# Kernel tuning notes

Measured on AMD Instinct MI355X. Metric: run time of the kernel, lower is better.

The kernel has to match this reference:

```python
import jax, jax.numpy as jnp
import numpy as np

B, C, L = 256, 512, 150
CI = C // 4            # channel_in = in_dim // 4 = 128
K = 150                # one_hot_cls_num (depthwise kernel over length)
POOL = 150             # MaxPool2d kernel (150, 1)
EPS = 1e-5             # BatchNorm eps


def setup_inputs() -> dict:
    key = jax.random.key(0)
    ks = jax.random.split(key, 8)
    n = lambda k, shape, s: jax.random.normal(k, shape, jnp.float32) * s
    return {
        "x":    jax.random.normal(ks[0], (B, C, L, 1), jnp.float32),
        "Wv":   n(ks[1], (CI, C), 0.06),   "bv": jnp.zeros((CI,), jnp.float32),
        "Wq":   n(ks[2], (CI, CI), 0.12),  "bq": jnp.zeros((CI,), jnp.float32),
        "Wk":   n(ks[3], (CI, CI), 0.12),  "bk": jnp.zeros((CI,), jnp.float32),
        "gamma": n(ks[4], (), 1.0),
        "Wd":   n(ks[5], (2 * CI, K), 0.1), "bd": jnp.zeros((2 * CI,), jnp.float32),
        "Wp":   n(ks[6], (2 * CI, 2 * CI), 0.08), "bp": jnp.zeros((2 * CI,), jnp.float32),
        "bn_g": jnp.ones((2 * CI,), jnp.float32),
        "bn_b": jnp.zeros((2 * CI,), jnp.float32),
    }


def reference(x, Wv, bv, Wq, bq, Wk, bk, gamma, Wd, bd, Wp, bp, bn_g, bn_b):
    xb = x[..., 0]                                             # [B, C, L] (trailing width==1)
    # 1x1 convs are per-position matmuls over the channel dim
    v = jnp.einsum('oc,bcl->bol', Wv, xb) + bv[:, None]        # [B, CI, L]
    q = jnp.einsum('oc,bcl->bol', Wq, v) + bq[:, None]         # [B, CI, L]
    k = jnp.einsum('oc,bcl->bol', Wk, v) + bk[:, None]         # [B, CI, L]
    # raw (unscaled) attention: energy = q^T k, softmax over keys
    energy = jnp.einsum('bci,bcj->bij', q, k)                  # [B, L, L]
    attn = jax.nn.softmax(energy, axis=-1)
    # x = bmm(v, attn^T): out[b,c,i] = sum_j v[b,c,j] * attn[b,i,j]
    att_out = jnp.einsum('bcj,bij->bci', v, attn)              # [B, CI, L]
    cat = jnp.concatenate([gamma * att_out, v], axis=1)        # [B, 2CI, L]
    # MaxPool2d kernel=(150,1), stride=(150,1) over length
    Lp = L // POOL
    y = cat[:, :, : Lp * POOL].reshape(B, 2 * CI, Lp, POOL).max(axis=-1)
    y = y.reshape(B, -1)                                       # [B, 2CI*Lp]
    # depthwise conv kernel (K,1), VALID padding, groups = 2CI
    dw = jax.lax.conv_general_dilated(
        cat[:, :, :, None],                                    # [B, 2CI, L, 1]
        Wd[:, None, :, None],                                  # [2CI, 1, K, 1]
        window_strides=(1, 1), padding='VALID',
        dimension_numbers=('NCHW', 'OIHW', 'NCHW'),
        feature_group_count=2 * CI,
    ) + bd[None, :, None, None]                                # [B, 2CI, L-K+1, 1]
    # pointwise 1x1 conv
    pw = jnp.einsum('oc,bchw->bohw', Wp, dw) + bp[None, :, None, None]
    # BatchNorm2d in training mode: per-channel batch stats (biased variance)
    mean = pw.mean(axis=(0, 2, 3))
    var = pw.var(axis=(0, 2, 3))
    xn = (pw - mean[None, :, None, None]) * jax.lax.rsqrt(var[None, :, None, None] + EPS)
    out = jax.nn.relu(xn * bn_g[None, :, None, None] + bn_b[None, :, None, None])
    return jnp.concatenate([out.reshape(B, -1), y], axis=1)    # [B, 2CI*(L-K+1) + 2CI*Lp]
```

## Files before the change

kernel.cpp:

```cpp
#include <hip/hip_runtime.h>


typedef float f32x4  __attribute__((ext_vector_type(4)));
typedef float f32x16 __attribute__((ext_vector_type(16)));
typedef short s16x8  __attribute__((ext_vector_type(8)));
typedef unsigned short BF;

union U8 { s16x8 v; BF u[8]; uint2 d[2]; unsigned w[4]; };

__device__ __forceinline__ BF bfhi(float f) { return (BF)(__float_as_uint(f) >> 16); }
__device__ __forceinline__ float bff(BF h) { return __uint_as_float(((unsigned)h) << 16); }
__device__ __forceinline__ BF bflo(float f, BF hi) { return bfhi(f - bff(hi)); }
__device__ __forceinline__ BF bfrne(float f) {
    unsigned u = __float_as_uint(f);
    u += 0x7fffu + ((u >> 16) & 1u);
    return (BF)(u >> 16);
}
__device__ __forceinline__ s16x8 ld8l(const BF* p) {
    U8 t; t.d[0] = *(const uint2*)p; t.d[1] = *(const uint2*)(p + 4); return t.v;
}
__device__ __forceinline__ void st4(BF* p, BF a, BF b, BF c, BF d) {
    uint2 t; t.x = (unsigned)a | ((unsigned)b << 16);
    t.y = (unsigned)c | ((unsigned)d << 16);
    *(uint2*)p = t;
}
__device__ __forceinline__ void ldv8(const unsigned* p, s16x8& hi, s16x8& lo) {
    unsigned u[8];
    *(uint4*)&u[0] = *(const uint4*)p;
    *(uint4*)&u[4] = *(const uint4*)(p + 4);
    U8 H, L;
    #pragma unroll
    for (int e = 0; e < 4; ++e) {
        unsigned a = u[2*e], b2 = u[2*e + 1];
        H.w[e] = (a >> 16) | (b2 & 0xffff0000u);
        L.w[e] = (a & 0xffffu) | (b2 << 16);
    }
    hi = H.v; lo = L.v;
}
#define MFMA(a, b, c)   __builtin_amdgcn_mfma_f32_16x16x32_bf16(a, b, c, 0, 0, 0)
#define MFMA32(a, b, c) __builtin_amdgcn_mfma_f32_32x32x16_bf16(a, b, c, 0, 0, 0)

__global__ __launch_bounds__(256)
void prep_all(const float* __restrict__ Wv, const float* __restrict__ Wq,
              const float* __restrict__ Wk, const float* __restrict__ bq,
              BF* __restrict__ wvh, BF* __restrict__ wvl,
              BF* __restrict__ wqh, BF* __restrict__ wql,
              float* __restrict__ cvec)
{
    __shared__ float qs[128][33], ks_[128][33];
    const int blk = blockIdx.x, tid = threadIdx.x;
    if (blk < 64) {
        int i = blk * 1024 + tid * 4;
        float4 v = *(const float4*)(Wv + i);
        BF h0 = bfhi(v.x), h1 = bfhi(v.y), h2 = bfhi(v.z), h3 = bfhi(v.w);
        st4(&wvh[i], h0, h1, h2, h3);
        st4(&wvl[i], bflo(v.x,h0), bflo(v.y,h1), bflo(v.z,h2), bflo(v.w,h3));
    } else if (blk < 80) {
        int bi = blk - 64;
        int d1_0 = (bi >> 2) * 32, d2_0 = (bi & 3) * 32;
        for (int i = tid; i < 4096; i += 256) {
            int o = i >> 5, c = i & 31;
            qs[o][c]  = Wq[o * 128 + d1_0 + c];
            ks_[o][c] = Wk[o * 128 + d2_0 + c];
        }
        __syncthreads();
        #pragma unroll
        for (int j = 0; j < 4; ++j) {
            int idx = j * 256 + tid;
            int d1 = idx >> 5, d2 = idx & 31;
            float s = 0.f;
            #pragma unroll 8
            for (int o = 0; o < 128; ++o) s = fmaf(qs[o][d1], ks_[o][d2], s);
            BF h = bfhi(s);
            wqh[(d1_0 + d1) * 128 + d2_0 + d2] = h;
            wql[(d1_0 + d1) * 128 + d2_0 + d2] = bflo(s, h);
        }
    } else {
        if (tid < 128) {
            float s = 0.f;
            for (int o = 0; o < 128; ++o) s += bq[o] * Wk[o * 128 + tid];
            cvec[tid] = s;
        }
    }
}

__global__ __launch_bounds__(512, 4)
void k1_v(const float* __restrict__ x, const BF* __restrict__ wvh,
          const BF* __restrict__ wvl, const float* __restrict__ bv,
          const float* __restrict__ Wd,
          unsigned* __restrict__ vp, float* __restrict__ vpm,
          float* __restrict__ vpd)
{
    __shared__ BF xt[2][2][80][36];
    const int bx = blockIdx.x;
    const int b = bx & 255, lh = bx >> 8;
    const int l0 = lh * 80;
    const float* xb = x + (long)b * 76800 + l0;
    const int tid = threadIdx.x, lane = tid & 63, w = tid >> 6;
    const int li = lane & 15, gq = lane >> 4;

    if (w < 4) {
        f32x4 acc[5][2];
        #pragma unroll
        for (int mf = 0; mf < 5; ++mf)
            #pragma unroll
            for (int nf = 0; nf < 2; ++nf) acc[mf][nf] = f32x4{0.f,0.f,0.f,0.f};
        s16x8 bh[2], bl[2];
        #pragma unroll
        for (int nf = 0; nf < 2; ++nf) {
            long g = (long)(w*32 + nf*16 + li)*512 + gq*8;
            bh[nf] = *(const s16x8*)(wvh + g);
            bl[nf] = *(const s16x8*)(wvl + g);
        }
        __syncthreads();
        for (int p = 0; p < 16; ++p) {
            s16x8 nbh[2], nbl[2];
            if (p < 15) {
                #pragma unroll
                for (int nf = 0; nf < 2; ++nf) {
                    long g = (long)(w*32 + nf*16 + li)*512 + (p+1)*32 + gq*8;
                    nbh[nf] = *(const s16x8*)(wvh + g);
                    nbl[nf] = *(const s16x8*)(wvl + g);
                }
            }
            const BF (*xh)[36] = xt[p & 1][0];
            const BF (*xl)[36] = xt[p & 1][1];
            #pragma unroll
            for (int mf = 0; mf < 5; ++mf) {
                int row = mf*16 + li;
                s16x8 ah = ld8l(&xh[row][gq*8]);
                s16x8 al = ld8l(&xl[row][gq*8]);
                #pragma unroll
                for (int nf = 0; nf < 2; ++nf) {
                    acc[mf][nf] = MFMA(al, bh[nf], acc[mf][nf]);
                    acc[mf][nf] = MFMA(ah, bl[nf], acc[mf][nf]);
                    acc[mf][nf] = MFMA(ah, bh[nf], acc[mf][nf]);
                }
            }
            if (p < 15) {
                #pragma unroll
                for (int nf = 0; nf < 2; ++nf) { bh[nf] = nbh[nf]; bl[nf] = nbl[nf]; }
            }
            __syncthreads();
        }
        #pragma unroll
        for (int nf = 0; nf < 2; ++nf) {
            int c = w*32 + nf*16 + li;
            float bvv = bv[c];
            float mx = -3.4e38f, dt = 0.f;
            #pragma unroll
            for (int mf = 0; mf < 5; ++mf)
                #pragma unroll
                for (int r = 0; r < 4; ++r) {
                    int ll = mf*16 + gq*4 + r;
                    float f = acc[mf][nf][r] + bvv;
                    BF h = bfhi(f);
                    BF lo2 = bflo(f, h);
                    vp[((long)b*160 + l0 + ll)*128 + c] = ((unsigned)h << 16) | lo2;
                    if (l0 + ll < 150) {
                        mx = fmaxf(mx, f);
                        dt = fmaf(f, Wd[(128 + c)*150 + l0 + ll], dt);
                    }
                }
            mx = fmaxf(mx, __shfl_xor(mx, 16)); dt += __shfl_xor(dt, 16);
            mx = fmaxf(mx, __shfl_xor(mx, 32)); dt += __shfl_xor(dt, 32);
            if (gq == 0) {
                vpm[((long)lh*256 + b)*128 + c] = mx;
                vpd[((long)lh*256 + b)*128 + c] = dt;
            }
        }
    } else {
        const int sw = w - 4;
        const int bound = (lh == 0) ? 16 : 6;
        float cur[2][8];
        auto ldchunk = [&](int p) {
            #pragma unroll
            for (int cc = 0; cc < 8; ++cc) {
                int ch = p*32 + sw*8 + cc;
                cur[0][cc] = xb[ch*150 + lane];
                cur[1][cc] = (lane < bound) ? xb[ch*150 + 64 + lane] : 0.f;
            }
        };
        auto wrchunk = [&](int buf) {
            #pragma unroll
            for (int g2 = 0; g2 < 2; ++g2) {
                BF h0 = bfhi(cur[0][g2*4+0]), h1 = bfhi(cur[0][g2*4+1]);
                BF h2 = bfhi(cur[0][g2*4+2]), h3 = bfhi(cur[0][g2*4+3]);
                st4(&xt[buf][0][lane][sw*8 + g2*4], h0, h1, h2, h3);
                st4(&xt[buf][1][lane][sw*8 + g2*4],
                    bflo(cur[0][g2*4+0],h0), bflo(cur[0][g2*4+1],h1),
                    bflo(cur[0][g2*4+2],h2), bflo(cur[0][g2*4+3],h3));
                if (lane < 16) {
                    BF k0 = bfhi(cur[1][g2*4+0]), k1 = bfhi(cur[1][g2*4+1]);
                    BF k2 = bfhi(cur[1][g2*4+2]), k3 = bfhi(cur[1][g2*4+3]);
                    st4(&xt[buf][0][64 + lane][sw*8 + g2*4], k0, k1, k2, k3);
                    st4(&xt[buf][1][64 + lane][sw*8 + g2*4],
                        bflo(cur[1][g2*4+0],k0), bflo(cur[1][g2*4+1],k1),
                        bflo(cur[1][g2*4+2],k2), bflo(cur[1][g2*4+3],k3));
                }
            }
        };
        ldchunk(0); wrchunk(0); ldchunk(1);
        __syncthreads();
        for (int p = 0; p < 16; ++p) {
            if (p < 15) {
                wrchunk((p + 1) & 1);
                if (p < 14) ldchunk(p + 2);
            }
            __syncthreads();
        }
    }
}

__global__ __launch_bounds__(1024, 8)
void k2_attn(const unsigned* __restrict__ vp,
             const BF* __restrict__ wqh, const BF* __restrict__ wql,
             const float* __restrict__ cvec, const float* __restrict__ gammap,
             const float* __restrict__ Wd,
             const float* __restrict__ vpm, const float* __restrict__ vpd,
             float* __restrict__ dw, float* __restrict__ out)
{
    __shared__ char smem[60672];
    BF (*ts)[2][192][36] = (BF(*)[2][192][36])smem;
    BF (*P)[172] = (BF(*)[172])smem;
    float* smax = (float*)(smem + 55296);
    float* ssum = smax + 480;
    float* svp  = ssum + 480;

    const int b = blockIdx.x;
    const unsigned* vb = vp + (long)b * 20480;
    const int tid = threadIdx.x;
    const int lane = tid & 63, w = tid >> 6;
    const int li = lane & 15, gq = lane >> 4;
    const int l31 = lane & 31, hi5 = lane >> 5;
    const float gamma = gammap[0];

    f32x4 eacc[2][4];
    #pragma unroll
    for (int a = 0; a < 2; ++a)
        #pragma unroll
        for (int b2 = 0; b2 < 4; ++b2) eacc[a][b2] = f32x4{0.f,0.f,0.f,0.f};
    const int iw = w / 3, jw = w % 3;

    for (int pr = 0; pr < 2; ++pr) {
        if (w < 10) {
            const int s2 = w / 5, jt = w % 5;
            const int ss = pr*2 + s2;
            f32x16 tacc;
            #pragma unroll
            for (int r = 0; r < 16; ++r) tacc[r] = 0.f;
            const unsigned* arow = vb + (jt*32 + l31)*128;
            const long brow = (long)(ss*32 + l31)*128;
            #pragma unroll
            for (int kc = 0; kc < 8; ++kc) {
                int kof = kc*16 + hi5*8;
                s16x8 bh = *(const s16x8*)(wqh + brow + kof);
                s16x8 bl = *(const s16x8*)(wql + brow + kof);
                s16x8 ah, al;
                ldv8(arow + kof, ah, al);
                tacc = MFMA32(al, bh, tacc);
                tacc = MFMA32(ah, bl, tacc);
                tacc = MFMA32(ah, bh, tacc);
            }
            #pragma unroll
            for (int r = 0; r < 16; ++r) {
                int j = jt*32 + (r & 3) + 8*(r >> 2) + 4*hi5;
                float f = tacc[r];
                BF h = bfhi(f);
                ts[s2][0][j][l31] = h;
                ts[s2][1][j][l31] = bflo(f, h);
            }
        } else if (pr == 0) {
            int t2 = tid - 640;
            unsigned* tz = (unsigned*)smem;
            for (int z = t2; z < 2304; z += 384) {
                int sb = z / 576, rz = z % 576;
                tz[(sb*192 + 160)*18 + rz] = 0u;
            }
            int r = t2 >> 1, hf = t2 & 1;
            if (r < 160) {
                const unsigned* vr = vb + r*128 + hf*64;
                float s = 0.f;
                #pragma unroll 8
                for (int d2 = 0; d2 < 64; ++d2)
                    s += cvec[hf*64 + d2] * bff((BF)(vr[d2] >> 16));
                svp[hf*192 + r] = s;
            }
        }
        __syncthreads();
        if (w < 15) {
            #pragma unroll
            for (int s2 = 0; s2 < 2; ++s2) {
                int scol = (pr*2 + s2)*32 + gq*8;
                s16x8 ah[2], al[2];
                #pragma unroll
                for (int mf2 = 0; mf2 < 2; ++mf2)
                    ldv8(vb + (iw*32 + mf2*16 + li)*128 + scol, ah[mf2], al[mf2]);
                #pragma unroll
                for (int nf = 0; nf < 4; ++nf) {
                    int jr = jw*64 + nf*16 + li;
                    s16x8 bh = ld8l(&ts[s2][0][jr][gq*8]);
                    s16x8 bl = ld8l(&ts[s2][1][jr][gq*8]);
                    #pragma unroll
                    for (int mf2 = 0; mf2 < 2; ++mf2) {
                        eacc[mf2][nf] = MFMA(ah[mf2], bh, eacc[mf2][nf]);
                        eacc[mf2][nf] = MFMA(ah[mf2], bl, eacc[mf2][nf]);
                        eacc[mf2][nf] = MFMA(al[mf2], bh, eacc[mf2][nf]);
                    }
                }
            }
        }
        __syncthreads();
    }

    if (w < 15) {
        #pragma unroll
        for (int nf = 0; nf < 4; ++nf) {
            int j = jw*64 + nf*16 + li;
            float sv = svp[j] + svp[192 + j];
            #pragma unroll
            for (int mf2 = 0; mf2 < 2; ++mf2)
                #pragma unroll
                for (int r = 0; r < 4; ++r)
                    eacc[mf2][nf][r] += sv;
        }
        #pragma unroll
        for (int mf2 = 0; mf2 < 2; ++mf2)
            #pragma unroll
            for (int r = 0; r < 4; ++r) {
                int i = iw*32 + mf2*16 + gq*4 + r;
                float m = -3.4e38f;
                #pragma unroll
                for (int nf = 0; nf < 4; ++nf) {
                    int j = jw*64 + nf*16 + li;
                    if (j < 150) m = fmaxf(m, eacc[mf2][nf][r]);
                }
                #pragma unroll
                for (int o = 1; o < 16; o <<= 1) m = fmaxf(m, __shfl_xor(m, o));
                if (li == 0) smax[jw*160 + i] = m;
            }
    }
    __syncthreads();
    if (w < 15) {
        #pragma unroll
        for (int mf2 = 0; mf2 < 2; ++mf2)
            #pragma unroll
            for (int r = 0; r < 4; ++r) {
                int i = iw*32 + mf2*16 + gq*4 + r;
                float gm = fmaxf(fmaxf(smax[i], smax[160 + i]), smax[320 + i]);
                float rs_ = 0.f;
                #pragma unroll
                for (int nf = 0; nf < 4; ++nf) {
                    int j = jw*64 + nf*16 + li;
                    float e = (j < 150) ? __expf(eacc[mf2][nf][r] - gm) : 0.f;
                    eacc[mf2][nf][r] = e;
                    rs_ += e;
                }
                #pragma unroll
                for (int o = 1; o < 16; o <<= 1) rs_ += __shfl_xor(rs_, o);
                if (li == 0) ssum[jw*160 + i] = rs_;
            }
    }
    __syncthreads();
    if (w < 15) {
        #pragma unroll
        for (int mf2 = 0; mf2 < 2; ++mf2)
            #pragma unroll
            for (int r = 0; r < 4; ++r) {
                int i = iw*32 + mf2*16 + gq*4 + r;
                float inv = 1.f / (ssum[i] + ssum[160 + i] + ssum[320 + i]);
                #pragma unroll
                for (int nf = 0; nf < 4; ++nf) {
                    int j = jw*64 + nf*16 + li;
                    if (j < 160) P[i][j] = bfrne(eacc[mf2][nf][r] * inv);
                }
            }
    }
    __syncthreads();

    {
        const int pc = w & 7, pi = w >> 3;
        f32x4 oacc[5];
        #pragma unroll
        for (int i = 0; i < 5; ++i) oacc[i] = f32x4{0.f,0.f,0.f,0.f};
        #pragma unroll
        for (int ks = 0; ks < 5; ++ks) {
            int c = pc*16 + li;
            int j0 = ks*32 + gq*8;
            U8 t;
            #pragma unroll
            for (int e = 0; e < 8; ++e)
                t.u[e] = (BF)(vb[(j0 + e)*128 + c] >> 16);
            #pragma unroll
            for (int nf2 = 0; nf2 < 5; ++nf2) {
                int ir = pi*80 + nf2*16 + li;
                s16x8 bp = ld8l(&P[ir][ks*32 + gq*8]);
                oacc[nf2] = MFMA(t.v, bp, oacc[nf2]);
            }
        }

        float* pmax = smax;
        float* pdot = ssum;
        #pragma unroll
        for (int r = 0; r < 4; ++r) {
            int c = pc*16 + gq*4 + r;
            float mx = -3.4e38f, dt = 0.f;
            #pragma unroll
            for (int nf2 = 0; nf2 < 5; ++nf2) {
                int l = pi*80 + nf2*16 + li;
                if (l < 150) {
                    float val = gamma * oacc[nf2][r];
                    mx = fmaxf(mx, val);
                    dt = fmaf(val, Wd[c*150 + l], dt);
                }
            }
            #pragma unroll
            for (int o = 1; o < 16; o <<= 1) {
                mx = fmaxf(mx, __shfl_xor(mx, o));
                dt += __shfl_xor(dt, o);
            }
            if (li == 0) { pmax[pi*128 + c] = mx; pdot[pi*128 + c] = dt; }
        }
        __syncthreads();
        if (tid < 128) {
            out[(long)b*512 + 256 + tid] = fmaxf(pmax[tid], pmax[128 + tid]);
            dw[b*256 + tid] = pdot[tid] + pdot[128 + tid];
        } else if (tid < 256) {
            int c2 = tid - 128;
            float m0 = vpm[(long)b*128 + c2];
            float m1 = vpm[(long)(256 + b)*128 + c2];
            out[(long)b*512 + 384 + c2] = fmaxf(m0, m1);
            dw[b*256 + 128 + c2] = vpd[(long)b*128 + c2] + vpd[(long)(256 + b)*128 + c2];
        }
    }
}

__global__ __launch_bounds__(256)
void tail_pwbn(const float* __restrict__ dw, const float* __restrict__ Wp,
               const float* __restrict__ bn_g, const float* __restrict__ bn_b,
               float* __restrict__ out)
{
    __shared__ float wp_s[256];
    __shared__ float rs[4], rs2[4];
    const int o = blockIdx.x, t = threadIdx.x;
    const int lane = t & 63, w = t >> 6;
    wp_s[t] = Wp[o * 256 + t];
    __syncthreads();
    const float4* dr = (const float4*)(dw + (long)t * 256);
    float acc = 0.f;
    #pragma unroll 8
    for (int i = 0; i < 64; ++i) {
        float4 d4 = dr[i];
        acc = fmaf(d4.x, wp_s[i*4+0], acc);
        acc = fmaf(d4.y, wp_s[i*4+1], acc);
        acc = fmaf(d4.z, wp_s[i*4+2], acc);
        acc = fmaf(d4.w, wp_s[i*4+3], acc);
    }
    float s = acc, s2 = acc * acc;
    #pragma unroll
    for (int d = 1; d < 64; d <<= 1) { s += __shfl_xor(s, d); s2 += __shfl_xor(s2, d); }
    if (lane == 0) { rs[w] = s; rs2[w] = s2; }
    __syncthreads();
    float S  = rs[0] + rs[1] + rs[2] + rs[3];
    float S2 = rs2[0] + rs2[1] + rs2[2] + rs2[3];
    float mean = S * (1.f/256.f);
    float var  = S2 * (1.f/256.f) - mean * mean;
    float sc = rsqrtf(var + 1e-5f) * bn_g[o];
    float sh = bn_b[o] - mean * sc;
    out[(long)t * 512 + o] = fmaxf(fmaf(acc, sc, sh), 0.f);
}

extern "C" void kernel_launch(void* const* d_in, const int* in_sizes, int n_in,
                              void* d_out, int out_size, void* d_ws, size_t ws_size,
                              hipStream_t stream)
{
    (void)in_sizes; (void)n_in; (void)out_size; (void)ws_size;
    const float* x    = (const float*)d_in[0];
    const float* Wv   = (const float*)d_in[1];
    const float* bv   = (const float*)d_in[2];
    const float* Wq   = (const float*)d_in[3];
    const float* bq   = (const float*)d_in[4];
    const float* Wk   = (const float*)d_in[5];
    const float* bk   = (const float*)d_in[6];  (void)bk;
    const float* gam  = (const float*)d_in[7];
    const float* Wd   = (const float*)d_in[8];
    const float* Wp   = (const float*)d_in[10];
    const float* bn_g = (const float*)d_in[12];
    const float* bn_b = (const float*)d_in[13];
    float* out = (float*)d_out;

    char* wsb = (char*)d_ws;
    BF* wvh   = (BF*)wsb;
    BF* wvl   = (BF*)(wsb + 131072);
    BF* wqh   = (BF*)(wsb + 262144);
    BF* wql   = (BF*)(wsb + 294912);
    float* cvec = (float*)(wsb + 327680);
    unsigned* vpck = (unsigned*)(wsb + 328192);
    float* vpm  = (float*)(wsb + 21299712);
    float* vpd  = (float*)(wsb + 21561856);
    float* dw   = (float*)wsb;

    prep_all<<<81, 256, 0, stream>>>(Wv, Wq, Wk, bq, wvh, wvl, wqh, wql, cvec);
    k1_v<<<512, 512, 0, stream>>>(x, wvh, wvl, bv, Wd, vpck, vpm, vpd);
    k2_attn<<<256, 1024, 0, stream>>>(vpck, wqh, wql, cvec, gam, Wd, vpm, vpd,
                                      dw, out);
    tail_pwbn<<<256, 256, 0, stream>>>(dw, Wp, bn_g, bn_b, out);
}
```

Baseline: 107.7 us.

## Split k1 and k2 over length/query quarters, move svp to k1, add combine kernel

k1_v now processes 40-position quarters per block (1024 blocks) instead of 80-position halves, and it also computes the per-key bias term svg (v·cvec) that k2 used to compute. k2_attn is split across two query halves per batch (512 blocks), stores the transposed K operand as packed 32-bit hi/lo words, and computes the softmax in one pass with a per-segment max/sum merge. Per-half pooled max and depthwise dot partials go to global memory, and a new tail_comb kernel reduces them. The aim is more blocks for occupancy and less redundant work per block. In exchange it adds a kernel launch and extra global traffic, and each k2 block recomputes the K transpose for its half.

```diff
diff --git a/kernel.cpp b/kernel.cpp
--- a/kernel.cpp
+++ b/kernel.cpp
@@ -36,6 +36,10 @@
         L.w[e] = (a & 0xffffu) | (b2 << 16);
     }
     hi = H.v; lo = L.v;
+}
+__device__ __forceinline__ unsigned packf(float f) {
+    BF h = bfhi(f);
+    return ((unsigned)h << 16) | (unsigned)bflo(f, h);
 }
 #define MFMA(a, b, c)   __builtin_amdgcn_mfma_f32_16x16x32_bf16(a, b, c, 0, 0, 0)
 #define MFMA32(a, b, c) __builtin_amdgcn_mfma_f32_32x32x16_bf16(a, b, c, 0, 0, 0)
@@ -84,31 +88,34 @@
     }
 }
 
-__global__ __launch_bounds__(512, 4)
+__global__ __launch_bounds__(512, 8)
 void k1_v(const float* __restrict__ x, const BF* __restrict__ wvh,
           const BF* __restrict__ wvl, const float* __restrict__ bv,
-          const float* __restrict__ Wd,
-          unsigned* __restrict__ vp, float* __restrict__ vpm,
-          float* __restrict__ vpd)
+          const float* __restrict__ cvec, const float* __restrict__ Wd,
+          unsigned* __restrict__ vp, float* __restrict__ svg,
+          float* __restrict__ vpm, float* __restrict__ vpd)
 {
-    __shared__ BF xt[2][2][80][36];
+    __shared__ BF xt[2][2][48][40];
+    BF (*vhl)[132] = (BF(*)[132])&xt[0][0][0][0];
+
     const int bx = blockIdx.x;
-    const int b = bx & 255, lh = bx >> 8;
-    const int l0 = lh * 80;
-    const float* xb = x + (long)b * 76800 + l0;
+    const int b = bx & 255, lq = bx >> 8;
+    const int l0 = lq * 40;
+    const float* xb = x + (long)b * 76800;
     const int tid = threadIdx.x, lane = tid & 63, w = tid >> 6;
     const int li = lane & 15, gq = lane >> 4;
 
     if (w < 4) {
-        f32x4 acc[5][2];
-        #pragma unroll
-        for (int mf = 0; mf < 5; ++mf)
+        const int cw = w;
+        f32x4 acc[3][2];
+        #pragma unroll
+        for (int mf = 0; mf < 3; ++mf)
             #pragma unroll
             for (int nf = 0; nf < 2; ++nf) acc[mf][nf] = f32x4{0.f,0.f,0.f,0.f};
         s16x8 bh[2], bl[2];
         #pragma unroll
         for (int nf = 0; nf < 2; ++nf) {
-            long g = (long)(w*32 + nf*16 + li)*512 + gq*8;
+            long g = (long)(cw*32 + nf*16 + li)*512 + gq*8;
             bh[nf] = *(const s16x8*)(wvh + g);
             bl[nf] = *(const s16x8*)(wvl + g);
         }
@@ -118,18 +125,18 @@
             if (p < 15) {
                 #pragma unroll
                 for (int nf = 0; nf < 2; ++nf) {
-                    long g = (long)(w*32 + nf*16 + li)*512 + (p+1)*32 + gq*8;
+                    long g = (long)(cw*32 + nf*16 + li)*512 + (p+1)*32 + gq*8;
                     nbh[nf] = *(const s16x8*)(wvh + g);
                     nbl[nf] = *(const s16x8*)(wvl + g);
                 }
             }
-            const BF (*xh)[36] = xt[p & 1][0];
-            const BF (*xl)[36] = xt[p & 1][1];
-            #pragma unroll
-            for (int mf = 0; mf < 5; ++mf) {
+            const BF (*xh)[40] = xt[p & 1][0];
+            const BF (*xl)[40] = xt[p & 1][1];
+            #pragma unroll
+            for (int mf = 0; mf < 3; ++mf) {
                 int row = mf*16 + li;
-                s16x8 ah = ld8l(&xh[row][gq*8]);
-                s16x8 al = ld8l(&xl[row][gq*8]);
+                s16x8 ah = *(const s16x8*)&xh[row][gq*8];
+                s16x8 al = *(const s16x8*)&xl[row][gq*8];
                 #pragma unroll
                 for (int nf = 0; nf < 2; ++nf) {
                     acc[mf][nf] = MFMA(al, bh[nf], acc[mf][nf]);
@@ -145,58 +152,52 @@
         }
         #pragma unroll
         for (int nf = 0; nf < 2; ++nf) {
-            int c = w*32 + nf*16 + li;
+            int c = cw*32 + nf*16 + li;
             float bvv = bv[c];
             float mx = -3.4e38f, dt = 0.f;
             #pragma unroll
-            for (int mf = 0; mf < 5; ++mf)
+            for (int mf = 0; mf < 3; ++mf)
                 #pragma unroll
                 for (int r = 0; r < 4; ++r) {
                     int ll = mf*16 + gq*4 + r;
                     float f = acc[mf][nf][r] + bvv;
-                    BF h = bfhi(f);
-                    BF lo2 = bflo(f, h);
-                    vp[((long)b*160 + l0 + ll)*128 + c] = ((unsigned)h << 16) | lo2;
-                    if (l0 + ll < 150) {
-                        mx = fmaxf(mx, f);
-                        dt = fmaf(f, Wd[(128 + c)*150 + l0 + ll], dt);
+                    vhl[ll][c] = bfhi(f);
+                    if (ll < 40) {
+                        vp[((long)b*160 + l0 + ll)*128 + c] = packf(f);
+                        if (l0 + ll < 150) {
+                            mx = fmaxf(mx, f);
+                            dt = fmaf(f, Wd[(128 + c)*150 + l0 + ll], dt);
+                        }
                     }
                 }
             mx = fmaxf(mx, __shfl_xor(mx, 16)); dt += __shfl_xor(dt, 16);
             mx = fmaxf(mx, __shfl_xor(mx, 32)); dt += __shfl_xor(dt, 32);
             if (gq == 0) {
-                vpm[((long)lh*256 + b)*128 + c] = mx;
-                vpd[((long)lh*256 + b)*128 + c] = dt;
+                vpm[((long)lq*256 + b)*128 + c] = mx;
+                vpd[((long)lq*256 + b)*128 + c] = dt;
             }
         }
     } else {
         const int sw = w - 4;
-        const int bound = (lh == 0) ? 16 : 6;
-        float cur[2][8];
+        float cur[8];
+        const bool ok = (lane < 40) && (l0 + lane < 150);
         auto ldchunk = [&](int p) {
             #pragma unroll
             for (int cc = 0; cc < 8; ++cc) {
                 int ch = p*32 + sw*8 + cc;
-                cur[0][cc] = xb[ch*150 + lane];
-                cur[1][cc] = (lane < bound) ? xb[ch*150 + 64 + lane] : 0.f;
+                cur[cc] = ok ? xb[ch*150 + l0 + lane] : 0.f;
             }
         };
         auto wrchunk = [&](int buf) {
-            #pragma unroll
-            for (int g2 = 0; g2 < 2; ++g2) {
-                BF h0 = bfhi(cur[0][g2*4+0]), h1 = bfhi(cur[0][g2*4+1]);
-                BF h2 = bfhi(cur[0][g2*4+2]), h3 = bfhi(cur[0][g2*4+3]);
-                st4(&xt[buf][0][lane][sw*8 + g2*4], h0, h1, h2, h3);
-                st4(&xt[buf][1][lane][sw*8 + g2*4],
-                    bflo(cur[0][g2*4+0],h0), bflo(cur[0][g2*4+1],h1),
-                    bflo(cur[0][g2*4+2],h2), bflo(cur[0][g2*4+3],h3));
-                if (lane < 16) {
-                    BF k0 = bfhi(cur[1][g2*4+0]), k1 = bfhi(cur[1][g2*4+1]);
-                    BF k2 = bfhi(cur[1][g2*4+2]), k3 = bfhi(cur[1][g2*4+3]);
-                    st4(&xt[buf][0][64 + lane][sw*8 + g2*4], k0, k1, k2, k3);
-                    st4(&xt[buf][1][64 + lane][sw*8 + g2*4],
-                        bflo(cur[1][g2*4+0],k0), bflo(cur[1][g2*4+1],k1),
-                        bflo(cur[1][g2*4+2],k2), bflo(cur[1][g2*4+3],k3));
+            if (lane < 48) {
+                #pragma unroll
+                for (int g2 = 0; g2 < 2; ++g2) {
+                    BF h0 = bfhi(cur[g2*4+0]), h1 = bfhi(cur[g2*4+1]);
+                    BF h2 = bfhi(cur[g2*4+2]), h3 = bfhi(cur[g2*4+3]);
+                    st4(&xt[buf][0][lane][sw*8 + g2*4], h0, h1, h2, h3);
+                    st4(&xt[buf][1][lane][sw*8 + g2*4],
+                        bflo(cur[g2*4+0],h0), bflo(cur[g2*4+1],h1),
+                        bflo(cur[g2*4+2],h2), bflo(cur[g2*4+3],h3));
                 }
             }
         };
@@ -210,24 +211,37 @@
             __syncthreads();
         }
     }
+    __syncthreads();
+
+    if (tid < 320) {
+        int j = tid >> 3, ds = tid & 7;
+        float s = 0.f;
+        #pragma unroll
+        for (int k = 0; k < 16; ++k) {
+            int d = ds*16 + k;
+            s = fmaf(bff(vhl[j][d]), cvec[d], s);
+        }
+        s += __shfl_xor(s, 1); s += __shfl_xor(s, 2); s += __shfl_xor(s, 4);
+        if (ds == 0) svg[(long)b*160 + l0 + j] = s;
+    }
 }
 
 __global__ __launch_bounds__(1024, 8)
 void k2_attn(const unsigned* __restrict__ vp,
              const BF* __restrict__ wqh, const BF* __restrict__ wql,
-             const float* __restrict__ cvec, const float* __restrict__ gammap,
+             const float* __restrict__ svg, const float* __restrict__ gammap,
              const float* __restrict__ Wd,
-             const float* __restrict__ vpm, const float* __restrict__ vpd,
-             float* __restrict__ dw, float* __restrict__ out)
+             float* __restrict__ pmax_g, float* __restrict__ pdot_g)
 {
-    __shared__ char smem[60672];
-    BF (*ts)[2][192][36] = (BF(*)[2][192][36])smem;
-    BF (*P)[172] = (BF(*)[172])smem;
-    float* smax = (float*)(smem + 55296);
-    float* ssum = smax + 480;
-    float* svp  = ssum + 480;
-
-    const int b = blockIdx.x;
+    __shared__ char smem[69632];
+    unsigned (*ts32)[192][44] = (unsigned(*)[192][44])smem;
+    BF (*P)[168] = (BF(*)[168])smem;
+    float* mg = (float*)(smem + 67584);
+    float* sg = mg + 240;
+
+    const int bid = blockIdx.x;
+    const int b = bid & 255, ih = bid >> 8;
+    const int i0g = ih * 80;
     const unsigned* vb = vp + (long)b * 20480;
     const int tid = threadIdx.x;
     const int lane = tid & 63, w = tid >> 6;
@@ -235,12 +249,11 @@
     const int l31 = lane & 31, hi5 = lane >> 5;
     const float gamma = gammap[0];
 
-    f32x4 eacc[2][4];
+    const int iw = w / 3, jw = w % 3;
+
+    f32x4 eacc[4];
     #pragma unroll
-    for (int a = 0; a < 2; ++a)
-        #pragma unroll
-        for (int b2 = 0; b2 < 4; ++b2) eacc[a][b2] = f32x4{0.f,0.f,0.f,0.f};
-    const int iw = w / 3, jw = w % 3;
+    for (int i = 0; i < 4; ++i) eacc[i] = f32x4{0.f,0.f,0.f,0.f};
 
     for (int pr = 0; pr < 2; ++pr) {
         if (w < 10) {
@@ -265,26 +278,7 @@
             #pragma unroll
             for (int r = 0; r < 16; ++r) {
                 int j = jt*32 + (r & 3) + 8*(r >> 2) + 4*hi5;
-                float f = tacc[r];
-                BF h = bfhi(f);
-                ts[s2][0][j][l31] = h;
-                ts[s2][1][j][l31] = bflo(f, h);
-            }
-        } else if (pr == 0) {
-            int t2 = tid - 640;
-            unsigned* tz = (unsigned*)smem;
-            for (int z = t2; z < 2304; z += 384) {
-                int sb = z / 576, rz = z % 576;
-                tz[(sb*192 + 160)*18 + rz] = 0u;
-            }
-            int r = t2 >> 1, hf = t2 & 1;
-            if (r < 160) {
-                const unsigned* vr = vb + r*128 + hf*64;
-                float s = 0.f;
-                #pragma unroll 8
-                for (int d2 = 0; d2 < 64; ++d2)
-                    s += cvec[hf*64 + d2] * bff((BF)(vr[d2] >> 16));
-                svp[hf*192 + r] = s;
+                ts32[s2][j][l31] = packf(tacc[r]);
             }
         }
         __syncthreads();
@@ -292,21 +286,16 @@
             #pragma unroll
             for (int s2 = 0; s2 < 2; ++s2) {
                 int scol = (pr*2 + s2)*32 + gq*8;
-                s16x8 ah[2], al[2];
-                #pragma unroll
-                for (int mf2 = 0; mf2 < 2; ++mf2)
-                    ldv8(vb + (iw*32 + mf2*16 + li)*128 + scol, ah[mf2], al[mf2]);
+                s16x8 ah, al;
+                ldv8(vb + (long)(i0g + iw*16 + li)*128 + scol, ah, al);
                 #pragma unroll
                 for (int nf = 0; nf < 4; ++nf) {
                     int jr = jw*64 + nf*16 + li;
-                    s16x8 bh = ld8l(&ts[s2][0][jr][gq*8]);
-                    s16x8 bl = ld8l(&ts[s2][1][jr][gq*8]);
-                    #pragma unroll
-                    for (int mf2 = 0; mf2 < 2; ++mf2) {
-                        eacc[mf2][nf] = MFMA(ah[mf2], bh, eacc[mf2][nf]);
-                        eacc[mf2][nf] = MFMA(ah[mf2], bl, eacc[mf2][nf]);
-                        eacc[mf2][nf] = MFMA(al[mf2], bh, eacc[mf2][nf]);
-                    }
+                    s16x8 bh, bl;
+                    ldv8(&ts32[s2][jr][gq*8], bh, bl);
+                    eacc[nf] = MFMA(ah, bl, eacc[nf]);
+                    eacc[nf] = MFMA(al, bh, eacc[nf]);
+                    eacc[nf] = MFMA(ah, bh, eacc[nf]);
                 }
             }
         }
@@ -317,72 +306,61 @@
         #pragma unroll
         for (int nf = 0; nf < 4; ++nf) {
             int j = jw*64 + nf*16 + li;
-            float sv = svp[j] + svp[192 + j];
-            #pragma unroll
-            for (int mf2 = 0; mf2 < 2; ++mf2)
-                #pragma unroll
-                for (int r = 0; r < 4; ++r)
-                    eacc[mf2][nf][r] += sv;
-        }
-        #pragma unroll
-        for (int mf2 = 0; mf2 < 2; ++mf2)
-            #pragma unroll
-            for (int r = 0; r < 4; ++r) {
-                int i = iw*32 + mf2*16 + gq*4 + r;
-                float m = -3.4e38f;
-                #pragma unroll
-                for (int nf = 0; nf < 4; ++nf) {
-                    int j = jw*64 + nf*16 + li;
-                    if (j < 150) m = fmaxf(m, eacc[mf2][nf][r]);
-                }
-                #pragma unroll
-                for (int o = 1; o < 16; o <<= 1) m = fmaxf(m, __shfl_xor(m, o));
-                if (li == 0) smax[jw*160 + i] = m;
-            }
+            float sv = svg[(long)b*160 + j];
+            #pragma unroll
+            for (int r = 0; r < 4; ++r) eacc[nf][r] += sv;
+        }
+        #pragma unroll
+        for (int r = 0; r < 4; ++r) {
+            int il = iw*16 + gq*4 + r;
+            float m = -3.4e38f;
+            #pragma unroll
+            for (int nf = 0; nf < 4; ++nf) {
+                int j = jw*64 + nf*16 + li;
+                if (j < 150) m = fmaxf(m, eacc[nf][r]);
+            }
+            #pragma unroll
+            for (int o = 1; o < 16; o <<= 1) m = fmaxf(m, __shfl_xor(m, o));
+            float rs_ = 0.f;
+            #pragma unroll
+            for (int nf = 0; nf < 4; ++nf) {
+                int j = jw*64 + nf*16 + li;
+                float e = (j < 150) ? __expf(eacc[nf][r] - m) : 0.f;
+                eacc[nf][r] = e;
+                rs_ += e;
+            }
+            #pragma unroll
+            for (int o = 1; o < 16; o <<= 1) rs_ += __shfl_xor(rs_, o);
+            if (li == 0) { mg[jw*80 + il] = m; sg[jw*80 + il] = rs_; }
+        }
     }
     __syncthreads();
     if (w < 15) {
         #pragma unroll
-        for (int mf2 = 0; mf2 < 2; ++mf2)
-            #pragma unroll
-            for (int r = 0; r < 4; ++r) {
-                int i = iw*32 + mf2*16 + gq*4 + r;
-                float gm = fmaxf(fmaxf(smax[i], smax[160 + i]), smax[320 + i]);
-                float rs_ = 0.f;
-                #pragma unroll
-                for (int nf = 0; nf < 4; ++nf) {
-                    int j = jw*64 + nf*16 + li;
-                    float e = (j < 150) ? __expf(eacc[mf2][nf][r] - gm) : 0.f;
-                    eacc[mf2][nf][r] = e;
-                    rs_ += e;
-                }
-                #pragma unroll
-                for (int o = 1; o < 16; o <<= 1) rs_ += __shfl_xor(rs_, o);
-                if (li == 0) ssum[jw*160 + i] = rs_;
-            }
-    }
-    __syncthreads();
-    if (w < 15) {
-        #pragma unroll
-        for (int mf2 = 0; mf2 < 2; ++mf2)
-            #pragma unroll
-            for (int r = 0; r < 4; ++r) {
-                int i = iw*32 + mf2*16 + gq*4 + r;
-                float inv = 1.f / (ssum[i] + ssum[160 + i] + ssum[320 + i]);
-                #pragma unroll
-                for (int nf = 0; nf < 4; ++nf) {
-                    int j = jw*64 + nf*16 + li;
-                    if (j < 160) P[i][j] = bfrne(eacc[mf2][nf][r] * inv);
-                }
-            }
+        for (int r = 0; r < 4; ++r) {
+            int il = iw*16 + gq*4 + r;
+            float m0 = mg[il], m1 = mg[80 + il], m2 = mg[160 + il];
+            float M = fmaxf(fmaxf(m0, m1), m2);
+            float S = fmaf(sg[il], __expf(m0 - M),
+                      fmaf(sg[80 + il], __expf(m1 - M),
+                           sg[160 + il] * __expf(m2 - M)));
+            float scale = __expf(mg[jw*80 + il] - M) / S;
+            #pragma unroll
+            for (int nf = 0; nf < 4; ++nf) {
+                int j = jw*64 + nf*16 + li;
+                if (j < 160) P[il][j] = bfrne(eacc[nf][r] * scale);
+            }
+        }
     }
     __syncthreads();
 
     {
         const int pc = w & 7, pi = w >> 3;
-        f32x4 oacc[5];
-        #pragma unroll
-        for (int i = 0; i < 5; ++i) oacc[i] = f32x4{0.f,0.f,0.f,0.f};
+        const int nfc = pi ? 2 : 3;
+        const int ibase = pi * 48;
+        f32x4 oacc[3];
+        #pragma unroll
+        for (int i = 0; i < 3; ++i) oacc[i] = f32x4{0.f,0.f,0.f,0.f};
         #pragma unroll
         for (int ks = 0; ks < 5; ++ks) {
             int c = pc*16 + li;
@@ -390,24 +368,19 @@
             U8 t;
             #pragma unroll
             for (int e = 0; e < 8; ++e)
-                t.u[e] = (BF)(vb[(j0 + e)*128 + c] >> 16);
-            #pragma unroll
-            for (int nf2 = 0; nf2 < 5; ++nf2) {
-                int ir = pi*80 + nf2*16 + li;
+                t.u[e] = (BF)(vb[(long)(j0 + e)*128 + c] >> 16);
+            for (int nf2 = 0; nf2 < nfc; ++nf2) {
+                int ir = ibase + nf2*16 + li;
                 s16x8 bp = ld8l(&P[ir][ks*32 + gq*8]);
                 oacc[nf2] = MFMA(t.v, bp, oacc[nf2]);
             }
         }
-
-        float* pmax = smax;
-        float* pdot = ssum;
         #pragma unroll
         for (int r = 0; r < 4; ++r) {
             int c = pc*16 + gq*4 + r;
             float mx = -3.4e38f, dt = 0.f;
-            #pragma unroll
-            for (int nf2 = 0; nf2 < 5; ++nf2) {
-                int l = pi*80 + nf2*16 + li;
+            for (int nf2 = 0; nf2 < nfc; ++nf2) {
+                int l = i0g + ibase + nf2*16 + li;
                 if (l < 150) {
                     float val = gamma * oacc[nf2][r];
                     mx = fmaxf(mx, val);
@@ -419,19 +392,40 @@
                 mx = fmaxf(mx, __shfl_xor(mx, o));
                 dt += __shfl_xor(dt, o);
             }
-            if (li == 0) { pmax[pi*128 + c] = mx; pdot[pi*128 + c] = dt; }
-        }
-        __syncthreads();
-        if (tid < 128) {
-            out[(long)b*512 + 256 + tid] = fmaxf(pmax[tid], pmax[128 + tid]);
-            dw[b*256 + tid] = pdot[tid] + pdot[128 + tid];
-        } else if (tid < 256) {
-            int c2 = tid - 128;
-            float m0 = vpm[(long)b*128 + c2];
-            float m1 = vpm[(long)(256 + b)*128 + c2];
-            out[(long)b*512 + 384 + c2] = fmaxf(m0, m1);
-            dw[b*256 + 128 + c2] = vpd[(long)b*128 + c2] + vpd[(long)(256 + b)*128 + c2];
-        }
+            if (li == 0) {
+                long k = (long)(ih*2 + pi)*256 + b;
+                pmax_g[k*128 + c] = mx;
+                pdot_g[k*128 + c] = dt;
+            }
+        }
+    }
+}
+
+__global__ __launch_bounds__(256)
+void tail_comb(const float* __restrict__ pmax_g, const float* __restrict__ pdot_g,
+               const float* __restrict__ vpm, const float* __restrict__ vpd,
+               float* __restrict__ dw, float* __restrict__ out)
+{
+    const int b = blockIdx.x, ch = threadIdx.x;
+    if (ch < 128) {
+        float mx = -3.4e38f, dt = 0.f;
+        #pragma unroll
+        for (int k = 0; k < 4; ++k) {
+            mx = fmaxf(mx, pmax_g[((long)k*256 + b)*128 + ch]);
+            dt += pdot_g[((long)k*256 + b)*128 + ch];
+        }
+        out[(long)b*512 + 256 + ch] = mx;
+        dw[b*256 + ch] = dt;
+    } else {
+        int c2 = ch - 128;
+        float mx = -3.4e38f, dt = 0.f;
+        #pragma unroll
+        for (int k = 0; k < 4; ++k) {
+            mx = fmaxf(mx, vpm[((long)k*256 + b)*128 + c2]);
+            dt += vpd[((long)k*256 + b)*128 + c2];
+        }
+        out[(long)b*512 + 256 + ch] = mx;
+        dw[b*256 + ch] = dt;
     }
 }
 
@@ -495,14 +489,17 @@
     BF* wqh   = (BF*)(wsb + 262144);
     BF* wql   = (BF*)(wsb + 294912);
     float* cvec = (float*)(wsb + 327680);
-    unsigned* vpck = (unsigned*)(wsb + 328192);
-    float* vpm  = (float*)(wsb + 21299712);
-    float* vpd  = (float*)(wsb + 21561856);
-    float* dw   = (float*)wsb;
+    float* svg  = (float*)(wsb + 328192);
+    unsigned* vpck = (unsigned*)(wsb + 492288);
+    float* vpm  = (float*)(wsb + 21463808);
+    float* vpd  = (float*)(wsb + 21988096);
+    float* pmax_g = (float*)(wsb + 22512384);
+    float* pdot_g = (float*)(wsb + 23036672);
+    float* dw   = (float*)(wsb + 23560960);
 
     prep_all<<<81, 256, 0, stream>>>(Wv, Wq, Wk, bq, wvh, wvl, wqh, wql, cvec);
-    k1_v<<<512, 512, 0, stream>>>(x, wvh, wvl, bv, Wd, vpck, vpm, vpd);
-    k2_attn<<<256, 1024, 0, stream>>>(vpck, wqh, wql, cvec, gam, Wd, vpm, vpd,
-                                      dw, out);
+    k1_v<<<1024, 512, 0, stream>>>(x, wvh, wvl, bv, cvec, Wd, vpck, svg, vpm, vpd);
+    k2_attn<<<512, 1024, 0, stream>>>(vpck, wqh, wql, svg, gam, Wd, pmax_g, pdot_g);
+    tail_comb<<<256, 256, 0, stream>>>(pmax_g, pdot_g, vpm, vpd, dw, out);
     tail_pwbn<<<256, 256, 0, stream>>>(dw, Wp, bn_g, bn_b, out);
 }
```

Result: slower. 136.8 us (+27.1%).
